# Kernel tuning notes

Hardware: AMD Instinct MI355X
Metric: run time of the kernel (lower is better)

## Reference

```python
import jax, jax.numpy as jnp
import numpy as np

N_HEAD = 4
IN_FEAT = 512
N_FEAT = 512
D_K = N_FEAT // N_HEAD
KERNEL = 11
SANM_SHIFT = 0
LEFT_PAD = (KERNEL - 1) // 2 + SANM_SHIFT
RIGHT_PAD = KERNEL - 1 - LEFT_PAD
B, T = 16, 1024
NEG = -1e9  # stand-in for -inf (grad-safe)


def setup_inputs() -> dict:
    key = jax.random.key(0)
    ks = jax.random.split(key, 6)
    x = jax.random.normal(ks[0], (B, T, IN_FEAT), dtype=jnp.float32)
    # padding mask: first 3/4 of frames valid, tail padded (as in batched ASR)
    valid = (jnp.arange(T) < (3 * T) // 4).astype(jnp.float32)
    mask = jnp.broadcast_to(valid[None, None, :], (B, 1, T))
    s = 1.0 / np.sqrt(IN_FEAT)
    w_qkv = jax.random.uniform(ks[1], (IN_FEAT, 3 * N_FEAT), jnp.float32, -s, s)
    b_qkv = jnp.zeros((3 * N_FEAT,), jnp.float32)
    so = 1.0 / np.sqrt(N_FEAT)
    w_out = jax.random.uniform(ks[2], (N_FEAT, N_FEAT), jnp.float32, -so, so)
    b_out = jnp.zeros((N_FEAT,), jnp.float32)
    # depthwise Conv1d weight: (channels, k)
    w_fsmn = jax.random.uniform(ks[3], (N_FEAT, KERNEL), jnp.float32, -1.0 / np.sqrt(KERNEL), 1.0 / np.sqrt(KERNEL))
    return {"x": x, "mask": mask, "w_qkv": w_qkv, "b_qkv": b_qkv,
            "w_out": w_out, "b_out": b_out, "w_fsmn": w_fsmn}


def _fsmn(v, mask_bt1, w_fsmn):
    # v: (B,T,D); mask_bt1: (B,T,1)
    inp = v * mask_bt1
    xc = jnp.transpose(inp, (0, 2, 1))                      # (B,D,T)
    xc = jnp.pad(xc, ((0, 0), (0, 0), (LEFT_PAD, RIGHT_PAD)))
    y = jax.lax.conv_general_dilated(
        xc, w_fsmn[:, None, :], window_strides=(1,), padding='VALID',
        feature_group_count=N_FEAT, dimension_numbers=('NCH', 'OIH', 'NCH'))
    y = jnp.transpose(y, (0, 2, 1)) + inp                   # residual
    return y * mask_bt1                                     # re-zero padded frames


def _forward(x, mask, w_qkv, b_qkv, w_out, b_out, w_fsmn):
    b, t, _ = x.shape
    qkv = x @ w_qkv + b_qkv                                 # (B,T,3D)
    q, k, v = jnp.split(qkv, 3, axis=-1)
    qh = q.reshape(b, t, N_HEAD, D_K).transpose(0, 2, 1, 3) # (B,H,T,dk)
    kh = k.reshape(b, t, N_HEAD, D_K).transpose(0, 2, 1, 3)
    vh = v.reshape(b, t, N_HEAD, D_K).transpose(0, 2, 1, 3)

    fsmn_mem = _fsmn(v, mask.reshape(b, t, 1), w_fsmn)

    scale = D_K ** (-0.5)
    scores = jnp.einsum('bhqd,bhkd->bhqk', qh * scale, kh)  # (B,H,T,T)
    m0 = (mask[:, None, :, :] == 0)                         # (B,1,1,T)
    scores = jnp.where(m0, NEG, scores)
    attn = jax.nn.softmax(scores, axis=-1)
    attn = jnp.where(m0, 0.0, attn)
    ctx = jnp.einsum('bhqk,bhkd->bhqd', attn, vh)
    ctx = ctx.transpose(0, 2, 1, 3).reshape(b, t, N_FEAT)
    att_out = ctx @ w_out + b_out
    return att_out + fsmn_mem


def reference(x, mask, w_qkv, b_qkv, w_out, b_out, w_fsmn):
    return _forward(x, mask, w_qkv, b_qkv, w_out, b_out, w_fsmn)
```

## Files before the change

### kernel.cpp

```cpp
#include <hip/hip_runtime.h>
#include <stdint.h>

#define SCALE_Q 0.08838834764831845f
#define LOG2E 1.4426950408889634f
#define NEGBIG -1e30f

typedef __attribute__((ext_vector_type(4))) float f32x4;
typedef __attribute__((ext_vector_type(16))) float f32x16;
typedef __attribute__((ext_vector_type(8))) short s16x8;
typedef __attribute__((ext_vector_type(4))) unsigned u32x4;

static __device__ __forceinline__ unsigned short f2bf(float f) {
  unsigned int u = __builtin_bit_cast(unsigned int, f);
  u += 0x7FFFu + ((u >> 16) & 1u);
  return (unsigned short)(u >> 16);
}
static __device__ __forceinline__ float bf2f(unsigned short b) {
  unsigned int u = ((unsigned int)b) << 16;
  return __builtin_bit_cast(float, u);
}

static __device__ __forceinline__ unsigned cvt_pk_bf16(float lo, float hi) {
  unsigned r;
  asm("v_cvt_pk_bf16_f32 %0, %1, %2" : "=v"(r) : "v"(lo), "v"(hi));
  return r;
}

static __device__ __forceinline__ float xchg_max(float x) {
  float a = x, b = x;
  asm("v_permlane32_swap_b32 %0, %1" : "+v"(a), "+v"(b));
  return fmaxf(a, b);
}
static __device__ __forceinline__ float xchg_sum(float x) {
  float a = x, b = x;
  asm("v_permlane32_swap_b32 %0, %1" : "+v"(a), "+v"(b));
  return a + b;
}

static __device__ __forceinline__ float vmax16(const f32x16& v) {
  float a = fmaxf(fmaxf(fmaxf(v[0], v[1]), fmaxf(v[2], v[3])),
                  fmaxf(fmaxf(v[4], v[5]), fmaxf(v[6], v[7])));
  float b = fmaxf(fmaxf(fmaxf(v[8], v[9]), fmaxf(v[10], v[11])),
                  fmaxf(fmaxf(v[12], v[13]), fmaxf(v[14], v[15])));
  return fmaxf(a, b);
}

static __device__ __forceinline__ void gload16(const void* g, void* l) {
  __builtin_amdgcn_global_load_lds(
      (const __attribute__((address_space(1))) void*)g,
      (__attribute__((address_space(3))) void*)l, 16, 0, 0);
}

__global__ void k_convert_x(const float* __restrict__ x, unsigned short* __restrict__ xb) {
  int i = (blockIdx.x * 256 + threadIdx.x) * 8;
  const float4* p = reinterpret_cast<const float4*>(x + i);
  float4 a = p[0], b = p[1];
  s16x8 o;
  o[0] = f2bf(a.x); o[1] = f2bf(a.y); o[2] = f2bf(a.z); o[3] = f2bf(a.w);
  o[4] = f2bf(b.x); o[5] = f2bf(b.y); o[6] = f2bf(b.z); o[7] = f2bf(b.w);
  *reinterpret_cast<s16x8*>(xb + i) = o;
}

__global__ void k_transpose_bf(const float* __restrict__ w, unsigned short* __restrict__ wt, int Nd) {
  int gid = blockIdx.x * 256 + threadIdx.x;
  int n = gid >> 6;
  int k0 = (gid & 63) * 8;
  if (n >= Nd) return;
  s16x8 o;
#pragma unroll
  for (int j = 0; j < 8; ++j) o[j] = f2bf(w[(size_t)(k0 + j) * Nd + n]);
  *reinterpret_cast<s16x8*>(wt + (size_t)n * 512 + k0) = o;
}

template <int MODE>
__launch_bounds__(256, 2)
__global__ void k_gemm(const unsigned short* __restrict__ A,
                       const unsigned short* __restrict__ Bt,
                       const float* __restrict__ bias,
                       const float* __restrict__ mask,
                       const float* __restrict__ wf,
                       const unsigned short* __restrict__ vsrc,
                       unsigned short* __restrict__ qs, unsigned short* __restrict__ kbuf,
                       unsigned short* __restrict__ vbf, unsigned short* __restrict__ vt,
                       float* __restrict__ outp,
                       int tiles_n, int cpx) {
  __shared__ unsigned short smem[32768];
  int bid0 = blockIdx.x;
  int bid = (bid0 & 7) * cpx + (bid0 >> 3);
  int rb = bid / tiles_n, cb = bid % tiles_n;
  int tid = threadIdx.x;
  int w = tid >> 6, lane = tid & 63;
  int g = lane >> 4, ln = lane & 15;
  int wr = w >> 1, wc = w & 1;

  if constexpr (MODE == 0) {
    if (cb >= 4) {
      int b = (rb * 128) >> 10, t0 = (rb * 128) & 1023;
      const float* mb = mask + b * 1024 + t0;
      float a0 = mb[lane * 2], a1 = mb[lane * 2 + 1];
      if (__ballot(a0 != 0.f || a1 != 0.f) == 0ull) return;
    }
  }

  int sr = lane >> 3;
  int sc = lane & 7;

  auto stage = [&](int kb0, int bsel) {
    unsigned short* al = smem + bsel * 16384;
    unsigned short* bl = al + 8192;
#pragma unroll
    for (int it = 0; it < 4; ++it) {
      int r0 = it * 32 + w * 8;
      int r = r0 + sr;
      int cg = sc ^ (r & 7);
      gload16(A + (size_t)(rb * 128 + r) * 512 + kb0 + cg * 8, al + r0 * 64);
      gload16(Bt + (size_t)(cb * 128 + r) * 512 + kb0 + cg * 8, bl + r0 * 64);
    }
  };

  f32x4 acc[4][4] = {};

  stage(0, 0);
  __syncthreads();
  int cur = 0;
  for (int kt = 0; kt < 8; ++kt) {
    if (kt < 7) stage((kt + 1) * 64, cur ^ 1);
    const unsigned short* al = smem + cur * 16384;
    const unsigned short* bl = al + 8192;
#pragma unroll
    for (int kk = 0; kk < 2; ++kk) {
      s16x8 af[4], bf[4];
#pragma unroll
      for (int m = 0; m < 4; ++m) {
        int row = wr * 64 + m * 16 + ln;
        af[m] = *reinterpret_cast<const s16x8*>(al + row * 64 + (((kk * 4 + g) ^ (row & 7)) * 8));
      }
#pragma unroll
      for (int n = 0; n < 4; ++n) {
        int row = wc * 64 + n * 16 + ln;
        bf[n] = *reinterpret_cast<const s16x8*>(bl + row * 64 + (((kk * 4 + g) ^ (row & 7)) * 8));
      }
#pragma unroll
      for (int m = 0; m < 4; ++m)
#pragma unroll
        for (int n = 0; n < 4; ++n)
          acc[m][n] = __builtin_amdgcn_mfma_f32_16x16x32_bf16(af[m], bf[n], acc[m][n], 0, 0, 0);
    }
    __syncthreads();
    cur ^= 1;
  }

  int c0 = cb * 128;
  int R0 = rb * 128 + wr * 64;

  if constexpr (MODE == 0) {
#pragma unroll
    for (int m = 0; m < 4; ++m) {
#pragma unroll
      for (int n = 0; n < 4; ++n) {
        int col = c0 + wc * 64 + n * 16 + ln;
        int Rbase = R0 + m * 16 + g * 4;
        float bv = bias[col];
        int which = col >> 9;
        int h = (col >> 7) & 3;
        int d = col & 127;
        int b = Rbase >> 10, t0 = Rbase & 1023;
        if (which == 2) {
          unsigned short pk[4];
#pragma unroll
          for (int r = 0; r < 4; ++r) {
            float v = acc[m][n][r] + bv;
            pk[r] = f2bf(v);
            vbf[(size_t)(Rbase + r) * 512 + (col - 1024)] = pk[r];
          }
          uint2 uv;
          uv.x = (unsigned)pk[0] | ((unsigned)pk[1] << 16);
          uv.y = (unsigned)pk[2] | ((unsigned)pk[3] << 16);
          *reinterpret_cast<uint2*>(vt + ((size_t)((b * 4 + h) * 128 + d)) * 1024 + t0) = uv;
        } else {
          unsigned short* dst = (which == 0) ? qs : kbuf;
          float sc2 = (which == 0) ? (SCALE_Q * LOG2E) : 1.0f;
#pragma unroll
          for (int r = 0; r < 4; ++r) {
            int t = t0 + r;
            dst[((size_t)((b * 4 + h) * 1024 + t)) * 128 + d] = f2bf((acc[m][n][r] + bv) * sc2);
          }
        }
      }
    }
  } else {
    int b = (rb * 128) >> 10, tloc0 = (rb * 128) & 1023;
    unsigned short* vh = smem;
    float* wl = reinterpret_cast<float*>(smem + 18816);
    for (int idx = tid; idx < 138 * 16; idx += 256) {
      int i = idx >> 4, gc = idx & 15;
      int tl = tloc0 - 5 + i;
      s16x8 v8 = {};
      if (tl >= 0 && tl < 1024) {
        if (mask[b * 1024 + tl] != 0.f)
          v8 = *reinterpret_cast<const s16x8*>(vsrc + ((size_t)b * 1024 + tl) * 512 + c0 + gc * 8);
      }
      *reinterpret_cast<s16x8*>(vh + i * 136 + gc * 8) = v8;
    }
    if (tid < 128) {
#pragma unroll
      for (int j = 0; j < 11; ++j) wl[tid * 11 + j] = wf[(c0 + tid) * 11 + j];
    }
    __syncthreads();

#pragma unroll
    for (int m = 0; m < 4; ++m) {
      int Rbase = R0 + m * 16 + g * 4;
      int lrb = Rbase - rb * 128;
      float mk[4];
#pragma unroll
      for (int r = 0; r < 4; ++r) mk[r] = mask[b * 1024 + ((Rbase + r) & 1023)];
#pragma unroll
      for (int n = 0; n < 4; ++n) {
        int lc = wc * 64 + n * 16 + ln;
        int col = c0 + lc;
        float bv = bias[col];
        float win[14];
#pragma unroll
        for (int i = 0; i < 14; ++i) win[i] = bf2f(vh[(lrb + i) * 136 + lc]);
        float wj[11];
#pragma unroll
        for (int j = 0; j < 11; ++j) wj[j] = wl[lc * 11 + j];
#pragma unroll
        for (int r = 0; r < 4; ++r) {
          float conv = win[r + 5];
#pragma unroll
          for (int j = 0; j < 11; ++j) conv += wj[j] * win[r + j];
          size_t idx = (size_t)(Rbase + r) * 512 + col;
          outp[idx] = acc[m][n][r] + bv + conv * mk[r];
        }
      }
    }
  }
}

__launch_bounds__(512, 1)
__global__ void k_attn(const unsigned short* __restrict__ qs,
                       const unsigned short* __restrict__ kbuf,
                       const unsigned short* __restrict__ vt,
                       const float* __restrict__ mask,
                       unsigned short* __restrict__ ctx) {
  __shared__ unsigned short smem[2 * 32768];

  int bid0 = blockIdx.x;
  int bid = (bid0 & 7) * 32 + (bid0 >> 3);
  int qc = bid & 3;
  int bh = bid >> 2;
  int b = bh >> 2, h = bh & 3;
  int tid = threadIdx.x;
  int w = tid >> 6, l = tid & 63;
  int half = l >> 5, lq = l & 31;

  const unsigned short* kbase = kbuf + (size_t)bh * 1024 * 128;
  const unsigned short* vtbase = vt + (size_t)bh * 128 * 1024;
  const float* mbase = mask + b * 1024;

  s16x8 aq[8];
  {
    const unsigned short* qrow = qs + ((size_t)bh * 1024 + qc * 256 + w * 32 + lq) * 128 + half * 8;
#pragma unroll
    for (int c = 0; c < 8; ++c)
      aq[c] = *reinterpret_cast<const s16x8*>(qrow + c * 16);
  }

  s16x8 bone = {};
  bone[0] = (short)(half == 0 ? 0x3F80 : 0);

  f32x16 o[4] = {};
  float M = NEGBIG, L = 0.f;

  unsigned amask = 0;
  for (int kb = 0; kb < 8; ++kb) {
    float m0 = mbase[kb * 128 + l];
    float m1 = mbase[kb * 128 + 64 + l];
    if (__ballot((m0 != 0.f) || (m1 != 0.f)) != 0ull) amask |= (1u << kb);
  }

  auto stage = [&](int kb, int bsel) {
    unsigned short* kd = smem + bsel * 32768;
    unsigned short* vd = kd + 16384;
    int srl = l >> 4;
    int scl = l & 15;
#pragma unroll
    for (int it = 0; it < 4; ++it) {
      int r0 = it * 32 + w * 4;
      int r = r0 + srl;
      int cg = scl ^ (r & 15);
      gload16(kbase + (size_t)(kb * 128 + r) * 128 + cg * 8, kd + r0 * 128);
      gload16(vtbase + (size_t)r * 1024 + kb * 128 + cg * 8, vd + r0 * 128);
    }
  };

  unsigned rem = amask;
  int kb_cur = __ffs(rem) - 1; rem &= rem - 1;
  stage(kb_cur, 0);
  __syncthreads();
  int cur = 0;

  while (true) {
    int kb_next = rem ? (__ffs(rem) - 1) : -1;
    if (kb_next >= 0) { rem &= rem - 1; stage(kb_next, cur ^ 1); }

    unsigned short* kl = smem + cur * 32768;
    unsigned short* vl = kl + 16384;

    f32x16 s[4];
    __builtin_amdgcn_s_setprio(1);
#pragma unroll
    for (int kt = 0; kt < 4; ++kt) {
      float mv = mbase[kb_cur * 128 + kt * 32 + lq];
      s16x8 ba = {};
      ba[0] = (short)((half == 0 && mv == 0.f) ? (short)0xFF7F : 0);
      f32x16 z = {};
      s[kt] = __builtin_amdgcn_mfma_f32_32x32x16_bf16(ba, bone, z, 0, 0, 0);
      int row = kt * 32 + lq, rx = row & 15;
#pragma unroll
      for (int c = 0; c < 8; ++c) {
        s16x8 kf = *reinterpret_cast<const s16x8*>(kl + row * 128 + (((c * 2 + half) ^ rx) * 8));
        s[kt] = __builtin_amdgcn_mfma_f32_32x32x16_bf16(kf, aq[c], s[kt], 0, 0, 0);
      }
    }
    __builtin_amdgcn_s_setprio(0);

    float mx = fmaxf(fmaxf(vmax16(s[0]), vmax16(s[1])), fmaxf(vmax16(s[2]), vmax16(s[3])));
    mx = xchg_max(mx);
    float mnew = fmaxf(M, mx);
    float alpha = exp2f(M - mnew);
    M = mnew;
    float ls0 = 0.f, ls1 = 0.f, ls2 = 0.f, ls3 = 0.f;
#pragma unroll
    for (int kt = 0; kt < 4; ++kt) {
#pragma unroll
      for (int i = 0; i < 16; ++i) {
        float p = exp2f(s[kt][i] - M);
        s[kt][i] = p;
        if ((i & 3) == 0) ls0 += p; else if ((i & 3) == 1) ls1 += p;
        else if ((i & 3) == 2) ls2 += p; else ls3 += p;
      }
    }
    float ls = (ls0 + ls1) + (ls2 + ls3);
    ls = xchg_sum(ls);
    L = L * alpha + ls;
#pragma unroll
    for (int dt = 0; dt < 4; ++dt)
#pragma unroll
      for (int i = 0; i < 16; ++i) o[dt][i] *= alpha;

    __builtin_amdgcn_s_setprio(1);
#pragma unroll
    for (int kt = 0; kt < 4; ++kt) {
      unsigned w0 = cvt_pk_bf16(s[kt][0], s[kt][1]);
      unsigned w1 = cvt_pk_bf16(s[kt][2], s[kt][3]);
      unsigned w2 = cvt_pk_bf16(s[kt][4], s[kt][5]);
      unsigned w3 = cvt_pk_bf16(s[kt][6], s[kt][7]);
      unsigned w4 = cvt_pk_bf16(s[kt][8], s[kt][9]);
      unsigned w5 = cvt_pk_bf16(s[kt][10], s[kt][11]);
      unsigned w6 = cvt_pk_bf16(s[kt][12], s[kt][13]);
      unsigned w7 = cvt_pk_bf16(s[kt][14], s[kt][15]);
      asm("v_permlane32_swap_b32 %0, %1" : "+v"(w0), "+v"(w2));
      asm("v_permlane32_swap_b32 %0, %1" : "+v"(w1), "+v"(w3));
      asm("v_permlane32_swap_b32 %0, %1" : "+v"(w4), "+v"(w6));
      asm("v_permlane32_swap_b32 %0, %1" : "+v"(w5), "+v"(w7));
      u32x4 f0 = {w0, w1, w2, w3};
      u32x4 f1 = {w4, w5, w6, w7};
      s16x8 p0 = __builtin_bit_cast(s16x8, f0);
      s16x8 p1 = __builtin_bit_cast(s16x8, f1);
#pragma unroll
      for (int dt = 0; dt < 4; ++dt) {
        int row = dt * 32 + lq, rx = row & 15;
        s16x8 va = *reinterpret_cast<const s16x8*>(vl + row * 128 + (((kt * 4 + half) ^ rx) * 8));
        o[dt] = __builtin_amdgcn_mfma_f32_32x32x16_bf16(va, p0, o[dt], 0, 0, 0);
        s16x8 vb = *reinterpret_cast<const s16x8*>(vl + row * 128 + (((kt * 4 + 2 + half) ^ rx) * 8));
        o[dt] = __builtin_amdgcn_mfma_f32_32x32x16_bf16(vb, p1, o[dt], 0, 0, 0);
      }
    }
    __builtin_amdgcn_s_setprio(0);

    if (kb_next < 0) break;
    __syncthreads();
    kb_cur = kb_next; cur ^= 1;
  }

  float inv = 1.0f / L;
  __syncthreads();
  unsigned short* obuf = smem;
#pragma unroll
  for (int dt = 0; dt < 4; ++dt) {
#pragma unroll
    for (int g = 0; g < 4; ++g) {
      int d0 = dt * 32 + g * 8 + half * 4;
      unsigned lo = cvt_pk_bf16(o[dt][g * 4 + 0] * inv, o[dt][g * 4 + 1] * inv);
      unsigned hi = cvt_pk_bf16(o[dt][g * 4 + 2] * inv, o[dt][g * 4 + 3] * inv);
      int row = w * 32 + lq;
      int gr = d0 >> 2;
      uint2 uv; uv.x = lo; uv.y = hi;
      *reinterpret_cast<uint2*>(obuf + row * 128 + ((gr ^ (row & 15)) * 4)) = uv;
    }
  }
  __syncthreads();
  size_t cbase = ((size_t)b * 1024 + qc * 256) * 512 + h * 128;
#pragma unroll
  for (int it = 0; it < 16; ++it) {
    int chunk = it * 512 + tid;
    int row = chunk >> 5, gr = chunk & 31;
    uint2 v = *reinterpret_cast<uint2*>(obuf + row * 128 + ((gr ^ (row & 15)) * 4));
    *reinterpret_cast<uint2*>(ctx + cbase + (size_t)row * 512 + gr * 4) = v;
  }
}

extern "C" void kernel_launch(void* const* d_in, const int* in_sizes, int n_in,
                              void* d_out, int out_size, void* d_ws, size_t ws_size,
                              hipStream_t stream) {
  const float* x      = (const float*)d_in[0];
  const float* mask   = (const float*)d_in[1];
  const float* w_qkv  = (const float*)d_in[2];
  const float* b_qkv  = (const float*)d_in[3];
  const float* w_out  = (const float*)d_in[4];
  const float* b_out  = (const float*)d_in[5];
  const float* w_fsmn = (const float*)d_in[6];
  float* out = (float*)d_out;

  char* ws = (char*)d_ws;
  size_t off = 0;
  auto alloc = [&](size_t bytes) { void* p = ws + off; off += (bytes + 255) & ~(size_t)255; return p; };
  unsigned short* x_bf   = (unsigned short*)alloc(16384ull * 512 * 2);
  unsigned short* wT_qkv = (unsigned short*)alloc(1536ull * 512 * 2);
  unsigned short* wT_out = (unsigned short*)alloc(512ull * 512 * 2);
  unsigned short* qs     = (unsigned short*)alloc(64ull * 1024 * 128 * 2);
  unsigned short* kbuf   = (unsigned short*)alloc(64ull * 1024 * 128 * 2);
  unsigned short* vt     = (unsigned short*)alloc(64ull * 128 * 1024 * 2);
  unsigned short* vbf    = (unsigned short*)alloc(16384ull * 512 * 2);
  unsigned short* ctx    = (unsigned short*)alloc(16384ull * 512 * 2);

  k_convert_x<<<4096, 256, 0, stream>>>(x, x_bf);
  k_transpose_bf<<<(1536 * 64) / 256, 256, 0, stream>>>(w_qkv, wT_qkv, 1536);
  k_transpose_bf<<<(512 * 64) / 256, 256, 0, stream>>>(w_out, wT_out, 512);
  k_gemm<0><<<128 * 12, 256, 0, stream>>>(x_bf, wT_qkv, b_qkv, mask, nullptr, nullptr,
                                          qs, kbuf, vbf, vt, nullptr, 12, (128 * 12) / 8);
  k_attn<<<256, 512, 0, stream>>>(qs, kbuf, vt, mask, ctx);
  k_gemm<1><<<128 * 4, 256, 0, stream>>>(ctx, wT_out, b_out, mask, w_fsmn, vbf,
                                         nullptr, nullptr, nullptr, nullptr, out, 4, (128 * 4) / 8);
}
```

Before: 205.0 us.

## Split attention KV across two wave groups, halve query tile, fuse prep kernels

The attention kernel now handles 128 query rows per block and splits the key/value blocks (now 64 wide) between two groups of four waves. Each group keeps its own online softmax, and the partial results are merged through shared memory at the end. The change also adds a lazy rescale that skips the alpha correction unless the max grows by more than 8, and lowers LDS use to allow more resident blocks. The three prep kernels are merged into one launch. The cost is removing the double-buffered prefetch, so loads and compute no longer overlap within a block and two barriers run per iteration.

```diff
diff --git a/kernel.cpp b/kernel.cpp
--- a/kernel.cpp
+++ b/kernel.cpp
@@ -51,25 +51,34 @@
       (__attribute__((address_space(3))) void*)l, 16, 0, 0);
 }
 
-__global__ void k_convert_x(const float* __restrict__ x, unsigned short* __restrict__ xb) {
-  int i = (blockIdx.x * 256 + threadIdx.x) * 8;
-  const float4* p = reinterpret_cast<const float4*>(x + i);
-  float4 a = p[0], b = p[1];
-  s16x8 o;
-  o[0] = f2bf(a.x); o[1] = f2bf(a.y); o[2] = f2bf(a.z); o[3] = f2bf(a.w);
-  o[4] = f2bf(b.x); o[5] = f2bf(b.y); o[6] = f2bf(b.z); o[7] = f2bf(b.w);
-  *reinterpret_cast<s16x8*>(xb + i) = o;
-}
-
-__global__ void k_transpose_bf(const float* __restrict__ w, unsigned short* __restrict__ wt, int Nd) {
-  int gid = blockIdx.x * 256 + threadIdx.x;
-  int n = gid >> 6;
-  int k0 = (gid & 63) * 8;
-  if (n >= Nd) return;
-  s16x8 o;
-#pragma unroll
-  for (int j = 0; j < 8; ++j) o[j] = f2bf(w[(size_t)(k0 + j) * Nd + n]);
-  *reinterpret_cast<s16x8*>(wt + (size_t)n * 512 + k0) = o;
+__global__ void k_prep(const float* __restrict__ x, unsigned short* __restrict__ xb,
+                       const float* __restrict__ w_qkv, unsigned short* __restrict__ wtq,
+                       const float* __restrict__ w_out, unsigned short* __restrict__ wto) {
+  int bid = blockIdx.x;
+  int tid = threadIdx.x;
+  if (bid < 4096) {
+    int i = (bid * 256 + tid) * 8;
+    const float4* p = reinterpret_cast<const float4*>(x + i);
+    float4 a = p[0], b = p[1];
+    s16x8 o;
+    o[0] = f2bf(a.x); o[1] = f2bf(a.y); o[2] = f2bf(a.z); o[3] = f2bf(a.w);
+    o[4] = f2bf(b.x); o[5] = f2bf(b.y); o[6] = f2bf(b.z); o[7] = f2bf(b.w);
+    *reinterpret_cast<s16x8*>(xb + i) = o;
+  } else if (bid < 4096 + 384) {
+    int gid = (bid - 4096) * 256 + tid;
+    int n = gid >> 6, k0 = (gid & 63) * 8;
+    s16x8 o;
+#pragma unroll
+    for (int j = 0; j < 8; ++j) o[j] = f2bf(w_qkv[(size_t)(k0 + j) * 1536 + n]);
+    *reinterpret_cast<s16x8*>(wtq + (size_t)n * 512 + k0) = o;
+  } else {
+    int gid = (bid - 4480) * 256 + tid;
+    int n = gid >> 6, k0 = (gid & 63) * 8;
+    s16x8 o;
+#pragma unroll
+    for (int j = 0; j < 8; ++j) o[j] = f2bf(w_out[(size_t)(k0 + j) * 512 + n]);
+    *reinterpret_cast<s16x8*>(wto + (size_t)n * 512 + k0) = o;
+  }
 }
 
 template <int MODE>
@@ -239,21 +248,22 @@
   }
 }
 
-__launch_bounds__(512, 1)
+__launch_bounds__(512, 4)
 __global__ void k_attn(const unsigned short* __restrict__ qs,
                        const unsigned short* __restrict__ kbuf,
                        const unsigned short* __restrict__ vt,
                        const float* __restrict__ mask,
                        unsigned short* __restrict__ ctx) {
-  __shared__ unsigned short smem[2 * 32768];
+  __shared__ unsigned short smem[33280];
 
   int bid0 = blockIdx.x;
-  int bid = (bid0 & 7) * 32 + (bid0 >> 3);
-  int qc = bid & 3;
-  int bh = bid >> 2;
+  int bid = (bid0 & 7) * 64 + (bid0 >> 3);
+  int qc = bid & 7;
+  int bh = bid >> 3;
   int b = bh >> 2, h = bh & 3;
   int tid = threadIdx.x;
   int w = tid >> 6, l = tid & 63;
+  int kvg = w >> 2, wq = w & 3, sw = w & 3;
   int half = l >> 5, lq = l & 31;
 
   const unsigned short* kbase = kbuf + (size_t)bh * 1024 * 128;
@@ -262,7 +272,7 @@
 
   s16x8 aq[8];
   {
-    const unsigned short* qrow = qs + ((size_t)bh * 1024 + qc * 256 + w * 32 + lq) * 128 + half * 8;
+    const unsigned short* qrow = qs + ((size_t)bh * 1024 + qc * 128 + wq * 32 + lq) * 128 + half * 8;
 #pragma unroll
     for (int c = 0; c < 8; ++c)
       aq[c] = *reinterpret_cast<const s16x8*>(qrow + c * 16);
@@ -275,137 +285,175 @@
   float M = NEGBIG, L = 0.f;
 
   unsigned amask = 0;
-  for (int kb = 0; kb < 8; ++kb) {
-    float m0 = mbase[kb * 128 + l];
-    float m1 = mbase[kb * 128 + 64 + l];
-    if (__ballot((m0 != 0.f) || (m1 != 0.f)) != 0ull) amask |= (1u << kb);
-  }
-
-  auto stage = [&](int kb, int bsel) {
-    unsigned short* kd = smem + bsel * 32768;
-    unsigned short* vd = kd + 16384;
-    int srl = l >> 4;
-    int scl = l & 15;
+  for (int kb = 0; kb < 16; ++kb) {
+    if (__ballot(mbase[kb * 64 + l] != 0.f) != 0ull) amask |= (1u << kb);
+  }
+
+  unsigned short* mybuf = smem + kvg * 16384;
+
+  auto stage4 = [&](int kb) {
+    unsigned short* kd = mybuf;
+    unsigned short* vd = mybuf + 8192;
+    int rk = l >> 4, ck = l & 15;
 #pragma unroll
     for (int it = 0; it < 4; ++it) {
-      int r0 = it * 32 + w * 4;
-      int r = r0 + srl;
-      int cg = scl ^ (r & 15);
-      gload16(kbase + (size_t)(kb * 128 + r) * 128 + cg * 8, kd + r0 * 128);
-      gload16(vtbase + (size_t)r * 1024 + kb * 128 + cg * 8, vd + r0 * 128);
+      int r0 = it * 16 + sw * 4;
+      int r = r0 + rk;
+      int cg = ck ^ (r & 15);
+      gload16(kbase + (size_t)(kb * 64 + r) * 128 + cg * 8, kd + r0 * 128);
+    }
+    int rv = l >> 3, cv = l & 7;
+#pragma unroll
+    for (int it = 0; it < 4; ++it) {
+      int r0 = it * 32 + sw * 8;
+      int r = r0 + rv;
+      int cg = cv ^ (r & 7);
+      gload16(vtbase + (size_t)r * 1024 + kb * 64 + cg * 8, vd + r0 * 64);
     }
   };
 
   unsigned rem = amask;
-  int kb_cur = __ffs(rem) - 1; rem &= rem - 1;
-  stage(kb_cur, 0);
+  while (rem) {
+    int kba = __ffs(rem) - 1; rem &= rem - 1;
+    int kbb = -1;
+    if (rem) { kbb = __ffs(rem) - 1; rem &= rem - 1; }
+    int mykb = kvg ? kbb : kba;
+
+    __syncthreads();
+    if (mykb >= 0) stage4(mykb);
+    __syncthreads();
+
+    if (mykb >= 0) {
+      const unsigned short* kl = mybuf;
+      const unsigned short* vl = mybuf + 8192;
+
+      f32x16 s[2];
+      __builtin_amdgcn_s_setprio(1);
+#pragma unroll
+      for (int kt = 0; kt < 2; ++kt) {
+        float mv = mbase[mykb * 64 + kt * 32 + lq];
+        s16x8 ba = {};
+        ba[0] = (short)((half == 0 && mv == 0.f) ? (short)0xFF7F : 0);
+        f32x16 z = {};
+        s[kt] = __builtin_amdgcn_mfma_f32_32x32x16_bf16(ba, bone, z, 0, 0, 0);
+        int row = kt * 32 + lq, rx = row & 15;
+#pragma unroll
+        for (int c = 0; c < 8; ++c) {
+          s16x8 kf = *reinterpret_cast<const s16x8*>(kl + row * 128 + (((c * 2 + half) ^ rx) * 8));
+          s[kt] = __builtin_amdgcn_mfma_f32_32x32x16_bf16(kf, aq[c], s[kt], 0, 0, 0);
+        }
+      }
+      __builtin_amdgcn_s_setprio(0);
+
+      float pmax = fmaxf(vmax16(s[0]), vmax16(s[1]));
+      pmax = xchg_max(pmax);
+      if (!__all(pmax <= M + 8.f)) {
+        float mnew = fmaxf(M, pmax);
+        float alpha = exp2f(M - mnew);
+        M = mnew;
+        L *= alpha;
+#pragma unroll
+        for (int dt = 0; dt < 4; ++dt)
+#pragma unroll
+          for (int i = 0; i < 16; ++i) o[dt][i] *= alpha;
+      }
+      float ls0 = 0.f, ls1 = 0.f, ls2 = 0.f, ls3 = 0.f;
+#pragma unroll
+      for (int kt = 0; kt < 2; ++kt) {
+#pragma unroll
+        for (int i = 0; i < 16; ++i) {
+          float p = exp2f(s[kt][i] - M);
+          s[kt][i] = p;
+          if ((i & 3) == 0) ls0 += p; else if ((i & 3) == 1) ls1 += p;
+          else if ((i & 3) == 2) ls2 += p; else ls3 += p;
+        }
+      }
+      float ls = (ls0 + ls1) + (ls2 + ls3);
+      ls = xchg_sum(ls);
+      L += ls;
+
+      __builtin_amdgcn_s_setprio(1);
+#pragma unroll
+      for (int kt = 0; kt < 2; ++kt) {
+        unsigned w0 = cvt_pk_bf16(s[kt][0], s[kt][1]);
+        unsigned w1 = cvt_pk_bf16(s[kt][2], s[kt][3]);
+        unsigned w2 = cvt_pk_bf16(s[kt][4], s[kt][5]);
+        unsigned w3 = cvt_pk_bf16(s[kt][6], s[kt][7]);
+        unsigned w4 = cvt_pk_bf16(s[kt][8], s[kt][9]);
+        unsigned w5 = cvt_pk_bf16(s[kt][10], s[kt][11]);
+        unsigned w6 = cvt_pk_bf16(s[kt][12], s[kt][13]);
+        unsigned w7 = cvt_pk_bf16(s[kt][14], s[kt][15]);
+        asm("v_permlane32_swap_b32 %0, %1" : "+v"(w0), "+v"(w2));
+        asm("v_permlane32_swap_b32 %0, %1" : "+v"(w1), "+v"(w3));
+        asm("v_permlane32_swap_b32 %0, %1" : "+v"(w4), "+v"(w6));
+        asm("v_permlane32_swap_b32 %0, %1" : "+v"(w5), "+v"(w7));
+        u32x4 f0 = {w0, w1, w2, w3};
+        u32x4 f1 = {w4, w5, w6, w7};
+        s16x8 p0 = __builtin_bit_cast(s16x8, f0);
+        s16x8 p1 = __builtin_bit_cast(s16x8, f1);
+#pragma unroll
+        for (int dt = 0; dt < 4; ++dt) {
+          int row = dt * 32 + lq, rx = row & 7;
+          s16x8 va = *reinterpret_cast<const s16x8*>(vl + row * 64 + (((kt * 4 + half) ^ rx) * 8));
+          o[dt] = __builtin_amdgcn_mfma_f32_32x32x16_bf16(va, p0, o[dt], 0, 0, 0);
+          s16x8 vb = *reinterpret_cast<const s16x8*>(vl + row * 64 + (((kt * 4 + 2 + half) ^ rx) * 8));
+          o[dt] = __builtin_amdgcn_mfma_f32_32x32x16_bf16(vb, p1, o[dt], 0, 0, 0);
+        }
+      }
+      __builtin_amdgcn_s_setprio(0);
+    }
+  }
+
   __syncthreads();
-  int cur = 0;
-
-  while (true) {
-    int kb_next = rem ? (__ffs(rem) - 1) : -1;
-    if (kb_next >= 0) { rem &= rem - 1; stage(kb_next, cur ^ 1); }
-
-    unsigned short* kl = smem + cur * 32768;
-    unsigned short* vl = kl + 16384;
-
-    f32x16 s[4];
-    __builtin_amdgcn_s_setprio(1);
-#pragma unroll
-    for (int kt = 0; kt < 4; ++kt) {
-      float mv = mbase[kb_cur * 128 + kt * 32 + lq];
-      s16x8 ba = {};
-      ba[0] = (short)((half == 0 && mv == 0.f) ? (short)0xFF7F : 0);
-      f32x16 z = {};
-      s[kt] = __builtin_amdgcn_mfma_f32_32x32x16_bf16(ba, bone, z, 0, 0, 0);
-      int row = kt * 32 + lq, rx = row & 15;
-#pragma unroll
-      for (int c = 0; c < 8; ++c) {
-        s16x8 kf = *reinterpret_cast<const s16x8*>(kl + row * 128 + (((c * 2 + half) ^ rx) * 8));
-        s[kt] = __builtin_amdgcn_mfma_f32_32x32x16_bf16(kf, aq[c], s[kt], 0, 0, 0);
-      }
-    }
-    __builtin_amdgcn_s_setprio(0);
-
-    float mx = fmaxf(fmaxf(vmax16(s[0]), vmax16(s[1])), fmaxf(vmax16(s[2]), vmax16(s[3])));
-    mx = xchg_max(mx);
-    float mnew = fmaxf(M, mx);
-    float alpha = exp2f(M - mnew);
-    M = mnew;
-    float ls0 = 0.f, ls1 = 0.f, ls2 = 0.f, ls3 = 0.f;
-#pragma unroll
-    for (int kt = 0; kt < 4; ++kt) {
+  float* oshare = reinterpret_cast<float*>(smem);
+  float* mlf = reinterpret_cast<float*>(smem) + 16384;
+  if (kvg == 1) {
+#pragma unroll
+    for (int dt = 0; dt < 4; ++dt)
 #pragma unroll
       for (int i = 0; i < 16; ++i) {
-        float p = exp2f(s[kt][i] - M);
-        s[kt][i] = p;
-        if ((i & 3) == 0) ls0 += p; else if ((i & 3) == 1) ls1 += p;
-        else if ((i & 3) == 2) ls2 += p; else ls3 += p;
-      }
-    }
-    float ls = (ls0 + ls1) + (ls2 + ls3);
-    ls = xchg_sum(ls);
-    L = L * alpha + ls;
+        int rowi = (i & 3) + 8 * (i >> 2) + 4 * half;
+        oshare[wq * 4096 + (dt * 32 + rowi) * 32 + lq] = o[dt][i];
+      }
+    if (half == 0) { mlf[wq * 64 + lq * 2] = M; mlf[wq * 64 + lq * 2 + 1] = L; }
+  }
+  __syncthreads();
+  if (kvg == 0) {
+    float M1 = mlf[wq * 64 + lq * 2], L1 = mlf[wq * 64 + lq * 2 + 1];
+    float mnew = fmaxf(M, M1);
+    float a0 = exp2f(M - mnew), a1 = exp2f(M1 - mnew);
+    L = L * a0 + L1 * a1;
 #pragma unroll
     for (int dt = 0; dt < 4; ++dt)
 #pragma unroll
-      for (int i = 0; i < 16; ++i) o[dt][i] *= alpha;
-
-    __builtin_amdgcn_s_setprio(1);
-#pragma unroll
-    for (int kt = 0; kt < 4; ++kt) {
-      unsigned w0 = cvt_pk_bf16(s[kt][0], s[kt][1]);
-      unsigned w1 = cvt_pk_bf16(s[kt][2], s[kt][3]);
-      unsigned w2 = cvt_pk_bf16(s[kt][4], s[kt][5]);
-      unsigned w3 = cvt_pk_bf16(s[kt][6], s[kt][7]);
-      unsigned w4 = cvt_pk_bf16(s[kt][8], s[kt][9]);
-      unsigned w5 = cvt_pk_bf16(s[kt][10], s[kt][11]);
-      unsigned w6 = cvt_pk_bf16(s[kt][12], s[kt][13]);
-      unsigned w7 = cvt_pk_bf16(s[kt][14], s[kt][15]);
-      asm("v_permlane32_swap_b32 %0, %1" : "+v"(w0), "+v"(w2));
-      asm("v_permlane32_swap_b32 %0, %1" : "+v"(w1), "+v"(w3));
-      asm("v_permlane32_swap_b32 %0, %1" : "+v"(w4), "+v"(w6));
-      asm("v_permlane32_swap_b32 %0, %1" : "+v"(w5), "+v"(w7));
-      u32x4 f0 = {w0, w1, w2, w3};
-      u32x4 f1 = {w4, w5, w6, w7};
-      s16x8 p0 = __builtin_bit_cast(s16x8, f0);
-      s16x8 p1 = __builtin_bit_cast(s16x8, f1);
-#pragma unroll
-      for (int dt = 0; dt < 4; ++dt) {
-        int row = dt * 32 + lq, rx = row & 15;
-        s16x8 va = *reinterpret_cast<const s16x8*>(vl + row * 128 + (((kt * 4 + half) ^ rx) * 8));
-        o[dt] = __builtin_amdgcn_mfma_f32_32x32x16_bf16(va, p0, o[dt], 0, 0, 0);
-        s16x8 vb = *reinterpret_cast<const s16x8*>(vl + row * 128 + (((kt * 4 + 2 + half) ^ rx) * 8));
-        o[dt] = __builtin_amdgcn_mfma_f32_32x32x16_bf16(vb, p1, o[dt], 0, 0, 0);
-      }
-    }
-    __builtin_amdgcn_s_setprio(0);
-
-    if (kb_next < 0) break;
-    __syncthreads();
-    kb_cur = kb_next; cur ^= 1;
-  }
-
-  float inv = 1.0f / L;
+      for (int i = 0; i < 16; ++i) {
+        int rowi = (i & 3) + 8 * (i >> 2) + 4 * half;
+        o[dt][i] = o[dt][i] * a0 + oshare[wq * 4096 + (dt * 32 + rowi) * 32 + lq] * a1;
+      }
+  }
   __syncthreads();
+
   unsigned short* obuf = smem;
-#pragma unroll
-  for (int dt = 0; dt < 4; ++dt) {
-#pragma unroll
-    for (int g = 0; g < 4; ++g) {
-      int d0 = dt * 32 + g * 8 + half * 4;
-      unsigned lo = cvt_pk_bf16(o[dt][g * 4 + 0] * inv, o[dt][g * 4 + 1] * inv);
-      unsigned hi = cvt_pk_bf16(o[dt][g * 4 + 2] * inv, o[dt][g * 4 + 3] * inv);
-      int row = w * 32 + lq;
-      int gr = d0 >> 2;
-      uint2 uv; uv.x = lo; uv.y = hi;
-      *reinterpret_cast<uint2*>(obuf + row * 128 + ((gr ^ (row & 15)) * 4)) = uv;
+  if (kvg == 0) {
+    float inv = (L > 0.f) ? 1.0f / L : 0.f;
+#pragma unroll
+    for (int dt = 0; dt < 4; ++dt) {
+#pragma unroll
+      for (int g = 0; g < 4; ++g) {
+        int d0 = dt * 32 + g * 8 + half * 4;
+        unsigned lo = cvt_pk_bf16(o[dt][g * 4 + 0] * inv, o[dt][g * 4 + 1] * inv);
+        unsigned hi = cvt_pk_bf16(o[dt][g * 4 + 2] * inv, o[dt][g * 4 + 3] * inv);
+        int row = wq * 32 + lq;
+        int gr = d0 >> 2;
+        uint2 uv; uv.x = lo; uv.y = hi;
+        *reinterpret_cast<uint2*>(obuf + row * 128 + ((gr ^ (row & 15)) * 4)) = uv;
+      }
     }
   }
   __syncthreads();
-  size_t cbase = ((size_t)b * 1024 + qc * 256) * 512 + h * 128;
-#pragma unroll
-  for (int it = 0; it < 16; ++it) {
+  size_t cbase = ((size_t)b * 1024 + qc * 128) * 512 + h * 128;
+#pragma unroll
+  for (int it = 0; it < 8; ++it) {
     int chunk = it * 512 + tid;
     int row = chunk >> 5, gr = chunk & 31;
     uint2 v = *reinterpret_cast<uint2*>(obuf + row * 128 + ((gr ^ (row & 15)) * 4));
@@ -437,12 +485,10 @@
   unsigned short* vbf    = (unsigned short*)alloc(16384ull * 512 * 2);
   unsigned short* ctx    = (unsigned short*)alloc(16384ull * 512 * 2);
 
-  k_convert_x<<<4096, 256, 0, stream>>>(x, x_bf);
-  k_transpose_bf<<<(1536 * 64) / 256, 256, 0, stream>>>(w_qkv, wT_qkv, 1536);
-  k_transpose_bf<<<(512 * 64) / 256, 256, 0, stream>>>(w_out, wT_out, 512);
+  k_prep<<<4608, 256, 0, stream>>>(x, x_bf, w_qkv, wT_qkv, w_out, wT_out);
   k_gemm<0><<<128 * 12, 256, 0, stream>>>(x_bf, wT_qkv, b_qkv, mask, nullptr, nullptr,
                                           qs, kbuf, vbf, vt, nullptr, 12, (128 * 12) / 8);
-  k_attn<<<256, 512, 0, stream>>>(qs, kbuf, vt, mask, ctx);
+  k_attn<<<512, 512, 0, stream>>>(qs, kbuf, vt, mask, ctx);
   k_gemm<1><<<128 * 4, 256, 0, stream>>>(ctx, wT_out, b_out, mask, w_fsmn, vbf,
                                          nullptr, nullptr, nullptr, nullptr, out, 4, (128 * 4) / 8);
 }
```

Result: slower. 321.8 us (+57.0%).
